# Performance work log

Measured on AMD Instinct MI355X. Metric: run time of the kernel, lower is better.

Reference implementation:

```python
import jax, jax.numpy as jnp
import numpy as np
import math

LN_EPS = 1e-5

def layer_norm(x, g, b):
    mu = jnp.mean(x, axis=-1, keepdims=True)
    var = jnp.mean(jnp.square(x - mu), axis=-1, keepdims=True)
    return (x - mu) * jax.lax.rsqrt(var + LN_EPS) * g + b

def positional_encoding(seq_len, d_model):
    pos = jnp.arange(seq_len, dtype=jnp.float32)[:, None]
    div = jnp.exp(jnp.arange(0, d_model, 2, dtype=jnp.float32) * (-math.log(10000.0) / d_model))
    ang = pos * div  # [S, D/2]
    # interleave: even indices sin, odd indices cos
    return jnp.stack([jnp.sin(ang), jnp.cos(ang)], axis=-1).reshape(seq_len, d_model)

def setup_inputs() -> dict:
    key = jax.random.key(0)
    V, D, H, L, F, B, S = 32000, 768, 12, 6, 3072, 4, 1024
    ks = jax.random.split(key, 12)
    s = 0.02
    inp = {
        'tokens': jax.random.randint(ks[0], (B, S), 0, V),
        'emb': jax.random.normal(ks[1], (V, D), jnp.float32) * s,
        'Wq': jax.random.normal(ks[2], (L, D, D), jnp.float32) * s,
        'bq': jnp.zeros((L, D), jnp.float32),
        'Wk': jax.random.normal(ks[3], (L, D, D), jnp.float32) * s,
        'bk': jnp.zeros((L, D), jnp.float32),
        'Wv': jax.random.normal(ks[4], (L, D, D), jnp.float32) * s,
        'bv': jnp.zeros((L, D), jnp.float32),
        'Wo': jax.random.normal(ks[5], (L, D, D), jnp.float32) * s,
        'bo': jnp.zeros((L, D), jnp.float32),
        'W1': jax.random.normal(ks[6], (L, D, F), jnp.float32) * s,
        'b1': jnp.zeros((L, F), jnp.float32),
        'W2': jax.random.normal(ks[7], (L, F, D), jnp.float32) * s,
        'b2': jnp.zeros((L, D), jnp.float32),
        'ln1_g': jnp.ones((L, D), jnp.float32), 'ln1_b': jnp.zeros((L, D), jnp.float32),
        'ln2_g': jnp.ones((L, D), jnp.float32), 'ln2_b': jnp.zeros((L, D), jnp.float32),
        'lnf_g': jnp.ones((D,), jnp.float32), 'lnf_b': jnp.zeros((D,), jnp.float32),
        'head_W': jax.random.normal(ks[8], (V, D), jnp.float32) * s,
    }
    return inp

def gpt_forward(tokens, emb, Wq, bq, Wk, bk, Wv, bv, Wo, bo, W1, b1, W2, b2,
                ln1_g, ln1_b, ln2_g, ln2_b, lnf_g, lnf_b, head_W):
    B, S = tokens.shape
    D = emb.shape[1]
    H = 12
    dk = D // H
    scale = 1.0 / math.sqrt(dk)
    causal = jnp.tril(jnp.ones((S, S), dtype=bool))  # [S,S]

    x = emb[tokens] + positional_encoding(S, D)  # [B,S,D]

    def block(x, p):
        wq, bq_, wk, bk_, wv, bv_, wo, bo_, w1, b1_, w2, b2_, g1, be1, g2, be2 = p
        h = layer_norm(x, g1, be1)
        q = (h @ wq + bq_).reshape(B, S, H, dk)
        k = (h @ wk + bk_).reshape(B, S, H, dk)
        v = (h @ wv + bv_).reshape(B, S, H, dk)
        scores = jnp.einsum('bqhd,bkhd->bhqk', q, k) * scale
        scores = jnp.where(causal, scores, -jnp.inf)
        attn = jax.nn.softmax(scores, axis=-1)
        o = jnp.einsum('bhqk,bkhd->bqhd', attn, v).reshape(B, S, D)
        x = x + o @ wo + bo_
        h2 = layer_norm(x, g2, be2)
        ff = jax.nn.gelu(h2 @ w1 + b1_, approximate=False) @ w2 + b2_
        x = x + ff
        return x, None

    layer_params = (Wq, bq, Wk, bk, Wv, bv, Wo, bo, W1, b1, W2, b2,
                    ln1_g, ln1_b, ln2_g, ln2_b)
    x, _ = jax.lax.scan(block, x, layer_params)
    x = layer_norm(x, lnf_g, lnf_b)
    logits = jnp.einsum('bsd,vd->bsv', x, head_W)  # head bias=False
    return logits

def reference(tokens, emb, Wq, bq, Wk, bk, Wv, bv, Wo, bo, W1, b1, W2, b2,
              ln1_g, ln1_b, ln2_g, ln2_b, lnf_g, lnf_b, head_W):
    return gpt_forward(tokens, emb, Wq, bq, Wk, bk, Wv, bv, Wo, bo, W1, b1, W2, b2,
                       ln1_g, ln1_b, ln2_g, ln2_b, lnf_g, lnf_b, head_W)
```

## Files before the change

kernel.cpp:

```cpp
#include <hip/hip_runtime.h>
#include <hip/hip_bf16.h>
#include <math.h>

#define BB 4
#define SS 1024
#define DD 768
#define HH 12
#define LL 6
#define FF 3072
#define VV 32000
#define DK 64
#define MM (BB * SS)

typedef __attribute__((ext_vector_type(8))) short s8v;
typedef __attribute__((ext_vector_type(4))) float f4v;

__device__ inline unsigned short f2bf_bits(float f) {
    unsigned u = __builtin_bit_cast(unsigned, f);
    unsigned r = (u + 0x7fffu + ((u >> 16) & 1u)) >> 16;
    return (unsigned short)r;
}

__device__ inline void gl_lds16(const void* g, void* l) {
    __builtin_amdgcn_global_load_lds((const __attribute__((address_space(1))) void*)g,
                                     (__attribute__((address_space(3))) void*)l, 16, 0, 0);
}

__global__ void embed_kernel(const int* __restrict__ tokens,
                             const float* __restrict__ emb,
                             float* __restrict__ x) {
    const int row = blockIdx.x;
    const int s = row % SS;
    const int tok = tokens[row];
    const float* er = emb + (size_t)tok * DD;
    float* xr = x + (size_t)row * DD;
    const float neg_ln_base = -logf(10000.0f) / (float)DD;
    for (int d = threadIdx.x; d < DD; d += blockDim.x) {
        int i2 = d & ~1;
        float div = expf((float)i2 * neg_ln_base);
        float ang = (float)s * div;
        float pe = (d & 1) ? cosf(ang) : sinf(ang);
        xr[d] = er[d] + pe;
    }
}

template <int OUTBF>
__global__ __launch_bounds__(256) void ln_kernel(const float* __restrict__ x,
                                                 const float* __restrict__ g,
                                                 const float* __restrict__ b,
                                                 void* __restrict__ outp) {
    const int row = blockIdx.x;
    const float* xr = x + (size_t)row * DD;
    float s = 0.f, s2 = 0.f;
    for (int d = threadIdx.x; d < DD; d += blockDim.x) {
        float v = xr[d];
        s += v; s2 += v * v;
    }
    __shared__ float rs[4], rs2[4];
    for (int off = 32; off; off >>= 1) {
        s  += __shfl_down(s, off);
        s2 += __shfl_down(s2, off);
    }
    const int wid = threadIdx.x >> 6;
    if ((threadIdx.x & 63) == 0) { rs[wid] = s; rs2[wid] = s2; }
    __syncthreads();
    s  = rs[0] + rs[1] + rs[2] + rs[3];
    s2 = rs2[0] + rs2[1] + rs2[2] + rs2[3];
    const float mu = s / (float)DD;
    const float var = s2 / (float)DD - mu * mu;
    const float r = rsqrtf(var + 1e-5f);
    for (int d = threadIdx.x; d < DD; d += blockDim.x) {
        float v = (xr[d] - mu) * r * g[d] + b[d];
        if (OUTBF) ((unsigned short*)outp)[(size_t)row * DD + d] = f2bf_bits(v);
        else       ((float*)outp)[(size_t)row * DD + d] = v;
    }
}

__global__ __launch_bounds__(256) void prep_kernel(const float* __restrict__ Wq,
                                                   const float* __restrict__ Wk,
                                                   const float* __restrict__ Wv,
                                                   const float* __restrict__ Wo,
                                                   const float* __restrict__ W1,
                                                   const float* __restrict__ W2,
                                                   unsigned short* __restrict__ wqkvT,
                                                   unsigned short* __restrict__ woT,
                                                   unsigned short* __restrict__ w1T,
                                                   unsigned short* __restrict__ w2T) {
    const int id = blockIdx.x;
    const float* src; unsigned short* dst; int R, C, t;
    if (id < 432)       { int seg = id / 144; t = id % 144;
                          src = (seg == 0 ? Wq : seg == 1 ? Wk : Wv);
                          dst = wqkvT + (size_t)seg * DD * DD; R = DD; C = DD; }
    else if (id < 576)  { t = id - 576 + 144; src = Wo; dst = woT; R = DD; C = DD; }
    else if (id < 1152) { t = id - 576;  src = W1; dst = w1T; R = DD; C = FF; }
    else                { t = id - 1152; src = W2; dst = w2T; R = FF; C = DD; }
    const int tilesC = C / 64;
    const int r0 = (t / tilesC) * 64, c0 = (t % tilesC) * 64;
    __shared__ float tb[64][65];
    const int lr = threadIdx.x >> 6, lc = threadIdx.x & 63;
    #pragma unroll
    for (int it = 0; it < 16; ++it) {
        int r = it * 4 + lr;
        tb[r][lc] = src[(size_t)(r0 + r) * C + c0 + lc];
    }
    __syncthreads();
    #pragma unroll
    for (int it = 0; it < 16; ++it) {
        int c = it * 4 + lr;
        dst[(size_t)(c0 + c) * R + r0 + lc] = f2bf_bits(tb[lc][c]);
    }
}

__global__ __launch_bounds__(256) void conv_kernel(const float* __restrict__ in,
                                                   unsigned short* __restrict__ out,
                                                   long n4) {
    long i = (long)blockIdx.x * 256 + threadIdx.x;
    if (i < n4) {
        float4 v = ((const float4*)in)[i];
        ushort4 o;
        o.x = f2bf_bits(v.x); o.y = f2bf_bits(v.y);
        o.z = f2bf_bits(v.z); o.w = f2bf_bits(v.w);
        ((ushort4*)out)[i] = o;
    }
}

template <int ACT, int RES, int OUTMODE>
__global__ __launch_bounds__(256) void gemm_mfma(const unsigned short* __restrict__ A,
                                                 const unsigned short* __restrict__ Bt,
                                                 const float* __restrict__ bias,
                                                 const float* res,
                                                 void* Cout, int M, int N, int K,
                                                 const float* biasK, const float* biasV,
                                                 unsigned short* kout, unsigned short* vtout) {
    __shared__ unsigned short As[128 * 32];
    __shared__ unsigned short Bs[128 * 32];
    const int tid = threadIdx.x;
    const int bm = blockIdx.y * 128, bn = blockIdx.x * 128;
    const int lane = tid & 63;
    const int wave = tid >> 6;
    const int wm = (wave >> 1) * 64, wn = (wave & 1) * 64;

    f4v acc[4][4];
    #pragma unroll
    for (int i = 0; i < 4; i++)
        #pragma unroll
        for (int j = 0; j < 4; j++)
            acc[i][j] = (f4v){0.f, 0.f, 0.f, 0.f};

    const int arow = tid >> 2;
    const int acol = (tid & 3) * 8;
    const unsigned short* gA0 = A  + (size_t)(bm + arow) * K + acol;
    const unsigned short* gA1 = gA0 + (size_t)64 * K;
    const unsigned short* gB0 = Bt + (size_t)(bn + arow) * K + acol;
    const unsigned short* gB1 = gB0 + (size_t)64 * K;
    char* lA0 = (char*)As + tid * 16;
    char* lA1 = lA0 + 4096;
    char* lB0 = (char*)Bs + tid * 16;
    char* lB1 = lB0 + 4096;

    const int fr = lane & 15;
    const int fk = (lane >> 4) * 8;

    for (int k0 = 0; k0 < K; k0 += 32) {
        gl_lds16(gA0 + k0, lA0);
        gl_lds16(gA1 + k0, lA1);
        gl_lds16(gB0 + k0, lB0);
        gl_lds16(gB1 + k0, lB1);
        __syncthreads();
        s8v af[4], bf[4];
        #pragma unroll
        for (int i = 0; i < 4; i++)
            af[i] = *(const s8v*)(As + (wm + i * 16 + fr) * 32 + fk);
        #pragma unroll
        for (int j = 0; j < 4; j++)
            bf[j] = *(const s8v*)(Bs + (wn + j * 16 + fr) * 32 + fk);
        #pragma unroll
        for (int i = 0; i < 4; i++)
            #pragma unroll
            for (int j = 0; j < 4; j++)
                acc[i][j] = __builtin_amdgcn_mfma_f32_16x16x32_bf16(af[i], bf[j], acc[i][j], 0, 0, 0);
        __syncthreads();
    }

    const int r0 = bm + wm + (lane >> 4) * 4;
    const int c0 = bn + wn + fr;
    #pragma unroll
    for (int i = 0; i < 4; i++) {
        const int rb = r0 + i * 16;
        #pragma unroll
        for (int j = 0; j < 4; j++) {
            const int c = c0 + j * 16;
            if (OUTMODE == 3) {
                const int seg = (c >= 1536) ? 2 : (c >= 768 ? 1 : 0);
                const int cc = c - seg * 768;
                const float bb = (seg == 0 ? bias[cc] : seg == 1 ? biasK[cc] : biasV[cc]);
                if (seg < 2) {
                    unsigned short* dst = (seg == 0 ? (unsigned short*)Cout : kout);
                    #pragma unroll
                    for (int q = 0; q < 4; q++)
                        dst[(size_t)(rb + q) * DD + cc] = f2bf_bits(acc[i][j][q] + bb);
                } else {
                    const int b_ = rb / SS, s_ = rb % SS;
                    const int h_ = cc >> 6, dd = cc & 63;
                    ushort4 pk;
                    pk.x = f2bf_bits(acc[i][j][0] + bb);
                    pk.y = f2bf_bits(acc[i][j][1] + bb);
                    pk.z = f2bf_bits(acc[i][j][2] + bb);
                    pk.w = f2bf_bits(acc[i][j][3] + bb);
                    *(ushort4*)(vtout + ((size_t)(b_ * HH + h_) * DK + dd) * SS + s_) = pk;
                }
            } else {
                const float bv = bias ? bias[c] : 0.f;
                #pragma unroll
                for (int q = 0; q < 4; q++) {
                    const int r = rb + q;
                    float v = acc[i][j][q] + bv;
                    if (ACT) v = 0.5f * v * (1.0f + erff(v * 0.70710678118654752f));
                    if (RES) v += res[(size_t)r * N + c];
                    if (OUTMODE == 1) ((unsigned short*)Cout)[(size_t)r * N + c] = f2bf_bits(v);
                    else              ((float*)Cout)[(size_t)r * N + c] = v;
                }
            }
        }
    }
}

__global__ __launch_bounds__(256) void fattn_kernel(const unsigned short* __restrict__ qb,
                                                    const unsigned short* __restrict__ kb,
                                                    const unsigned short* __restrict__ vt,
                                                    unsigned short* __restrict__ o) {
    __shared__ unsigned short Ks[64 * 64];
    __shared__ unsigned short Vs[64 * 64];
    __shared__ unsigned short Ps[4][16 * 64];

    const int qt = (int)gridDim.x - 1 - (int)blockIdx.x;
    const int bh = blockIdx.y;
    const int b = bh / HH, h = bh % HH;
    const int tid = threadIdx.x;
    const int lane = tid & 63;
    const int w = tid >> 6;
    const int fr = lane & 15;
    const int g  = lane >> 4;

    const int sr = tid >> 3;
    const int sc = tid & 7;
    const int scol = (sc * 8) ^ ((sr & 7) * 8);

    const int q0w = qt * 64 + w * 16;
    s8v qf[2];
    {
        const unsigned short* qrow = qb + (size_t)(b * SS + q0w + fr) * DD + h * DK + g * 8;
        qf[0] = *(const s8v*)(qrow);
        qf[1] = *(const s8v*)(qrow + 32);
    }

    f4v ofr[4];
    #pragma unroll
    for (int dj = 0; dj < 4; dj++) ofr[dj] = (f4v){0.f, 0.f, 0.f, 0.f};
    float mrow[4] = {-1e30f, -1e30f, -1e30f, -1e30f};
    float lrow[4] = {0.f, 0.f, 0.f, 0.f};

    unsigned short* Pw = &Ps[w][0];
    const int ktiles = qt + 1;

    for (int t = 0; t < ktiles; ++t) {
        const int k0 = t * 64;
        #pragma unroll
        for (int i = 0; i < 2; i++) {
            const int r = i * 32 + sr;
            gl_lds16(kb + (size_t)(b * SS + k0 + r) * DD + h * DK + scol,
                     (char*)Ks + i * 4096 + tid * 16);
            gl_lds16(vt + ((size_t)bh * DK + r) * SS + k0 + scol,
                     (char*)Vs + i * 4096 + tid * 16);
        }
        __syncthreads();

        f4v sfr[4];
        #pragma unroll
        for (int j = 0; j < 4; j++) {
            const char* kbase = (const char*)Ks + (j * 16 + fr) * 128;
            s8v b0 = *(const s8v*)(kbase + ((g * 16)      ^ ((fr & 7) << 4)));
            s8v b1 = *(const s8v*)(kbase + ((64 + g * 16) ^ ((fr & 7) << 4)));
            f4v a = (f4v){0.f, 0.f, 0.f, 0.f};
            a = __builtin_amdgcn_mfma_f32_16x16x32_bf16(qf[0], b0, a, 0, 0, 0);
            a = __builtin_amdgcn_mfma_f32_16x16x32_bf16(qf[1], b1, a, 0, 0, 0);
            sfr[j] = a;
        }

        const bool diag = (t == ktiles - 1);
        float p[4][4];
        #pragma unroll
        for (int j = 0; j < 4; j++)
            #pragma unroll
            for (int pq = 0; pq < 4; pq++) {
                float sv = sfr[j][pq] * 0.125f;
                if (diag && (k0 + j * 16 + fr > q0w + g * 4 + pq)) sv = -1e30f;
                p[j][pq] = sv;
            }

        float rmx[4];
        #pragma unroll
        for (int pq = 0; pq < 4; pq++)
            rmx[pq] = fmaxf(fmaxf(p[0][pq], p[1][pq]), fmaxf(p[2][pq], p[3][pq]));
        #pragma unroll
        for (int off = 1; off < 16; off <<= 1)
            #pragma unroll
            for (int pq = 0; pq < 4; pq++)
                rmx[pq] = fmaxf(rmx[pq], __shfl_xor(rmx[pq], off));

        float mnew[4], scf[4], rsum[4];
        #pragma unroll
        for (int pq = 0; pq < 4; pq++) {
            mnew[pq] = fmaxf(mrow[pq], rmx[pq]);
            scf[pq]  = __expf(mrow[pq] - mnew[pq]);
            rsum[pq] = 0.f;
        }
        #pragma unroll
        for (int j = 0; j < 4; j++)
            #pragma unroll
            for (int pq = 0; pq < 4; pq++) {
                float e = __expf(p[j][pq] - mnew[pq]);
                p[j][pq] = e;
                rsum[pq] += e;
            }
        #pragma unroll
        for (int off = 1; off < 16; off <<= 1)
            #pragma unroll
            for (int pq = 0; pq < 4; pq++)
                rsum[pq] += __shfl_xor(rsum[pq], off);
        #pragma unroll
        for (int pq = 0; pq < 4; pq++) {
            lrow[pq] = lrow[pq] * scf[pq] + rsum[pq];
            mrow[pq] = mnew[pq];
        }
        #pragma unroll
        for (int dj = 0; dj < 4; dj++)
            #pragma unroll
            for (int pq = 0; pq < 4; pq++)
                ofr[dj][pq] *= scf[pq];

        #pragma unroll
        for (int j = 0; j < 4; j++)
            #pragma unroll
            for (int pq = 0; pq < 4; pq++) {
                const int r = g * 4 + pq;
                *(unsigned short*)((char*)Pw + r * 128 + ((j * 32 + fr * 2) ^ ((r & 7) << 4))) =
                    f2bf_bits(p[j][pq]);
            }

        s8v pa0 = *(const s8v*)((const char*)Pw + fr * 128 + ((g * 16)       ^ ((fr & 7) << 4)));
        s8v pa1 = *(const s8v*)((const char*)Pw + fr * 128 + ((64 + g * 16)  ^ ((fr & 7) << 4)));
        #pragma unroll
        for (int dj = 0; dj < 4; dj++) {
            const char* vbase = (const char*)Vs + (dj * 16 + fr) * 128;
            s8v v0 = *(const s8v*)(vbase + ((g * 16)      ^ ((fr & 7) << 4)));
            s8v v1 = *(const s8v*)(vbase + ((64 + g * 16) ^ ((fr & 7) << 4)));
            ofr[dj] = __builtin_amdgcn_mfma_f32_16x16x32_bf16(pa0, v0, ofr[dj], 0, 0, 0);
            ofr[dj] = __builtin_amdgcn_mfma_f32_16x16x32_bf16(pa1, v1, ofr[dj], 0, 0, 0);
        }
        __syncthreads();
    }

    #pragma unroll
    for (int pq = 0; pq < 4; pq++) {
        const float inv = 1.0f / lrow[pq];
        const int row_abs = q0w + g * 4 + pq;
        #pragma unroll
        for (int dj = 0; dj < 4; dj++)
            o[(size_t)(b * SS + row_abs) * DD + h * DK + dj * 16 + fr] =
                f2bf_bits(ofr[dj][pq] * inv);
    }
}

extern "C" void kernel_launch(void* const* d_in, const int* in_sizes, int n_in,
                              void* d_out, int out_size, void* d_ws, size_t ws_size,
                              hipStream_t stream) {
    const int*   tokens = (const int*)d_in[0];
    const float* emb    = (const float*)d_in[1];
    const float* Wq     = (const float*)d_in[2];
    const float* bq     = (const float*)d_in[3];
    const float* Wk     = (const float*)d_in[4];
    const float* bk     = (const float*)d_in[5];
    const float* Wv     = (const float*)d_in[6];
    const float* bv     = (const float*)d_in[7];
    const float* Wo     = (const float*)d_in[8];
    const float* bo     = (const float*)d_in[9];
    const float* W1     = (const float*)d_in[10];
    const float* b1     = (const float*)d_in[11];
    const float* W2     = (const float*)d_in[12];
    const float* b2     = (const float*)d_in[13];
    const float* ln1_g  = (const float*)d_in[14];
    const float* ln1_b  = (const float*)d_in[15];
    const float* ln2_g  = (const float*)d_in[16];
    const float* ln2_b  = (const float*)d_in[17];
    const float* lnf_g  = (const float*)d_in[18];
    const float* lnf_b  = (const float*)d_in[19];
    const float* headW  = (const float*)d_in[20];
    float* out = (float*)d_out;
    (void)in_sizes; (void)n_in; (void)out_size; (void)ws_size;

    const size_t MD  = (size_t)MM * DD;
    const size_t MF  = (size_t)MM * FF;
    const size_t DxD = (size_t)DD * DD;
    const size_t DxF = (size_t)DD * FF;
    const size_t HWs = (size_t)VV * DD;

    char* p = (char*)d_ws;
    float*          x     = (float*)p;          p += MD * 4;
    unsigned short* qb    = (unsigned short*)p; p += MD * 2;
    unsigned short* kbuf  = (unsigned short*)p; p += MD * 2;
    unsigned short* vtb   = (unsigned short*)p; p += MD * 2;
    unsigned short* ao    = (unsigned short*)p; p += MD * 2;
    unsigned short* h     = (unsigned short*)p; p += MD * 2;
    unsigned short* mid   = (unsigned short*)p; p += MF * 2;
    unsigned short* wqkvT = (unsigned short*)p; p += 3 * DxD * 2;
    unsigned short* woT   = (unsigned short*)p; p += DxD * 2;
    unsigned short* w1T   = (unsigned short*)p; p += DxF * 2;
    unsigned short* w2T   = (unsigned short*)p; p += DxF * 2;
    unsigned short* hw    = (unsigned short*)p; p += HWs * 2;

    embed_kernel<<<MM, 256, 0, stream>>>(tokens, emb, x);
    conv_kernel<<<(int)((HWs / 4 + 255) / 256), 256, 0, stream>>>(headW, hw, (long)(HWs / 4));

    const dim3 gQKV(2304 / 128, MM / 128);
    const dim3 gD(DD * 2 / 256, MM / 128);
    const dim3 gF(FF / 128, MM / 128);
    const dim3 gV(VV / 128, MM / 128);
    const dim3 gA(SS / 64, BB * HH);

    for (int l = 0; l < LL; l++) {
        prep_kernel<<<1728, 256, 0, stream>>>(Wq + l * DxD, Wk + l * DxD, Wv + l * DxD,
                                              Wo + l * DxD, W1 + l * DxF, W2 + l * DxF,
                                              wqkvT, woT, w1T, w2T);
        ln_kernel<1><<<MM, 256, 0, stream>>>(x, ln1_g + l * DD, ln1_b + l * DD, h);
        gemm_mfma<0, 0, 3><<<gQKV, 256, 0, stream>>>(h, wqkvT, bq + l * DD, nullptr, qb,
                                                     MM, 2304, DD,
                                                     bk + l * DD, bv + l * DD, kbuf, vtb);
        fattn_kernel<<<gA, 256, 0, stream>>>(qb, kbuf, vtb, ao);
        gemm_mfma<0, 1, 0><<<gD, 256, 0, stream>>>(ao, woT, bo + l * DD, x, x, MM, DD, DD,
                                                   nullptr, nullptr, nullptr, nullptr);
        ln_kernel<1><<<MM, 256, 0, stream>>>(x, ln2_g + l * DD, ln2_b + l * DD, h);
        gemm_mfma<1, 0, 1><<<gF, 256, 0, stream>>>(h, w1T, b1 + l * FF, nullptr, mid,
                                                   MM, FF, DD, nullptr, nullptr, nullptr, nullptr);
        gemm_mfma<0, 1, 0><<<gD, 256, 0, stream>>>(mid, w2T, b2 + l * DD, x, x, MM, DD, FF,
                                                   nullptr, nullptr, nullptr, nullptr);
    }

    ln_kernel<1><<<MM, 256, 0, stream>>>(x, lnf_g, lnf_b, h);
    gemm_mfma<0, 0, 0><<<gV, 256, 0, stream>>>(h, hw, nullptr, nullptr, out, MM, VV, DD,
                                               nullptr, nullptr, nullptr, nullptr);
}
```

Measured before the change: 2.023 ms.

## Add dedicated 256x128 head GEMM and widen attention key tiles to 128

Adds a separate kernel for the large vocabulary projection. It uses 512 threads, 256x128 output tiles, a workgroup-id swizzle across groups of 8 and nontemporal stores for the large fp32 logits output. The flash-attention kernel now processes 128 keys per iteration instead of 64. That halves the loop trips and barriers per query tile, at the cost of more LDS and registers per block. The head kernel is single-buffered with K-step 32, so it relies on occupancy to hide load latency.

After: 1.870 ms. 7.6% less time.

```diff
diff --git a/kernel.cpp b/kernel.cpp
--- a/kernel.cpp
+++ b/kernel.cpp
@@ -225,13 +225,89 @@
     }
 }
 
+__global__ __launch_bounds__(512) void gemm_head(const unsigned short* __restrict__ A,
+                                                 const unsigned short* __restrict__ Bt,
+                                                 float* __restrict__ C,
+                                                 int M, int N, int K) {
+    __shared__ unsigned short As[256 * 32];
+    __shared__ unsigned short Bs[128 * 32];
+    const int tid = threadIdx.x;
+
+    const int nwg = gridDim.x * gridDim.y;
+    const int bid = blockIdx.y * gridDim.x + blockIdx.x;
+    const int cpx = nwg >> 3;
+    const int swz = (bid & 7) * cpx + (bid >> 3);
+    const int bx = swz % gridDim.x;
+    const int by = swz / gridDim.x;
+    const int bm = by * 256, bn = bx * 128;
+
+    const int lane = tid & 63;
+    const int wave = tid >> 6;
+    const int wm = (wave >> 1) * 64;
+    const int wn = (wave & 1) * 64;
+
+    f4v acc[4][4];
+    #pragma unroll
+    for (int i = 0; i < 4; i++)
+        #pragma unroll
+        for (int j = 0; j < 4; j++)
+            acc[i][j] = (f4v){0.f, 0.f, 0.f, 0.f};
+
+    const int arow = tid >> 2;
+    const int acol = (tid & 3) * 8;
+    const unsigned short* gA0 = A  + (size_t)(bm + arow) * K + acol;
+    const unsigned short* gA1 = gA0 + (size_t)128 * K;
+    const unsigned short* gB  = Bt + (size_t)(bn + arow) * K + acol;
+    char* lA0 = (char*)As + tid * 16;
+    char* lA1 = lA0 + 8192;
+    char* lB  = (char*)Bs + tid * 16;
+
+    const int fr = lane & 15;
+    const int fk = (lane >> 4) * 8;
+
+    for (int k0 = 0; k0 < K; k0 += 32) {
+        gl_lds16(gA0 + k0, lA0);
+        gl_lds16(gA1 + k0, lA1);
+        gl_lds16(gB + k0, lB);
+        __syncthreads();
+        s8v af[4], bf[4];
+        #pragma unroll
+        for (int i = 0; i < 4; i++)
+            af[i] = *(const s8v*)(As + (wm + i * 16 + fr) * 32 + fk);
+        #pragma unroll
+        for (int j = 0; j < 4; j++)
+            bf[j] = *(const s8v*)(Bs + (wn + j * 16 + fr) * 32 + fk);
+        #pragma unroll
+        for (int i = 0; i < 4; i++)
+            #pragma unroll
+            for (int j = 0; j < 4; j++)
+                acc[i][j] = __builtin_amdgcn_mfma_f32_16x16x32_bf16(af[i], bf[j], acc[i][j], 0, 0, 0);
+        __syncthreads();
+    }
+
+    const int r0 = bm + wm + (lane >> 4) * 4;
+    const int c0 = bn + wn + fr;
+    #pragma unroll
+    for (int i = 0; i < 4; i++) {
+        #pragma unroll
+        for (int j = 0; j < 4; j++) {
+            const int c = c0 + j * 16;
+            #pragma unroll
+            for (int q = 0; q < 4; q++) {
+                const int r = r0 + i * 16 + q;
+                __builtin_nontemporal_store(acc[i][j][q], &C[(size_t)r * N + c]);
+            }
+        }
+    }
+}
+
 __global__ __launch_bounds__(256) void fattn_kernel(const unsigned short* __restrict__ qb,
                                                     const unsigned short* __restrict__ kb,
                                                     const unsigned short* __restrict__ vt,
                                                     unsigned short* __restrict__ o) {
-    __shared__ unsigned short Ks[64 * 64];
-    __shared__ unsigned short Vs[64 * 64];
-    __shared__ unsigned short Ps[4][16 * 64];
+    __shared__ unsigned short Ks[128 * 64];
+    __shared__ unsigned short Vs[64 * 128];
+    __shared__ unsigned short Ps[4][16 * 128];
 
     const int qt = (int)gridDim.x - 1 - (int)blockIdx.x;
     const int bh = blockIdx.y;
@@ -242,9 +318,10 @@
     const int fr = lane & 15;
     const int g  = lane >> 4;
 
-    const int sr = tid >> 3;
-    const int sc = tid & 7;
-    const int scol = (sc * 8) ^ ((sr & 7) * 8);
+    const int krow_ = tid >> 3;
+    const int kcol = (((tid & 7) ^ (krow_ & 7)) * 8);
+    const int vrow_ = tid >> 4;
+    const int vcol = (((tid & 15) ^ (vrow_ & 7)) * 8);
 
     const int q0w = qt * 64 + w * 16;
     s8v qf[2];
@@ -261,47 +338,49 @@
     float lrow[4] = {0.f, 0.f, 0.f, 0.f};
 
     unsigned short* Pw = &Ps[w][0];
-    const int ktiles = qt + 1;
+    const int ktiles = qt / 2 + 1;
 
     for (int t = 0; t < ktiles; ++t) {
-        const int k0 = t * 64;
-        #pragma unroll
-        for (int i = 0; i < 2; i++) {
-            const int r = i * 32 + sr;
-            gl_lds16(kb + (size_t)(b * SS + k0 + r) * DD + h * DK + scol,
+        const int k0 = t * 128;
+        #pragma unroll
+        for (int i = 0; i < 4; i++) {
+            const int r = i * 32 + krow_;
+            gl_lds16(kb + (size_t)(b * SS + k0 + r) * DD + h * DK + kcol,
                      (char*)Ks + i * 4096 + tid * 16);
-            gl_lds16(vt + ((size_t)bh * DK + r) * SS + k0 + scol,
+        }
+        #pragma unroll
+        for (int i = 0; i < 4; i++) {
+            const int d = i * 16 + vrow_;
+            gl_lds16(vt + ((size_t)bh * DK + d) * SS + k0 + vcol,
                      (char*)Vs + i * 4096 + tid * 16);
         }
         __syncthreads();
 
-        f4v sfr[4];
-        #pragma unroll
-        for (int j = 0; j < 4; j++) {
+        const bool diag = (t == ktiles - 1);
+        float p[8][4];
+        #pragma unroll
+        for (int j = 0; j < 8; j++) {
             const char* kbase = (const char*)Ks + (j * 16 + fr) * 128;
             s8v b0 = *(const s8v*)(kbase + ((g * 16)      ^ ((fr & 7) << 4)));
             s8v b1 = *(const s8v*)(kbase + ((64 + g * 16) ^ ((fr & 7) << 4)));
             f4v a = (f4v){0.f, 0.f, 0.f, 0.f};
             a = __builtin_amdgcn_mfma_f32_16x16x32_bf16(qf[0], b0, a, 0, 0, 0);
             a = __builtin_amdgcn_mfma_f32_16x16x32_bf16(qf[1], b1, a, 0, 0, 0);
-            sfr[j] = a;
-        }
-
-        const bool diag = (t == ktiles - 1);
-        float p[4][4];
-        #pragma unroll
-        for (int j = 0; j < 4; j++)
             #pragma unroll
             for (int pq = 0; pq < 4; pq++) {
-                float sv = sfr[j][pq] * 0.125f;
+                float sv = a[pq] * 0.125f;
                 if (diag && (k0 + j * 16 + fr > q0w + g * 4 + pq)) sv = -1e30f;
                 p[j][pq] = sv;
             }
+        }
 
         float rmx[4];
         #pragma unroll
-        for (int pq = 0; pq < 4; pq++)
-            rmx[pq] = fmaxf(fmaxf(p[0][pq], p[1][pq]), fmaxf(p[2][pq], p[3][pq]));
+        for (int pq = 0; pq < 4; pq++) {
+            float v0 = fmaxf(fmaxf(p[0][pq], p[1][pq]), fmaxf(p[2][pq], p[3][pq]));
+            float v1 = fmaxf(fmaxf(p[4][pq], p[5][pq]), fmaxf(p[6][pq], p[7][pq]));
+            rmx[pq] = fmaxf(v0, v1);
+        }
         #pragma unroll
         for (int off = 1; off < 16; off <<= 1)
             #pragma unroll
@@ -316,7 +395,7 @@
             rsum[pq] = 0.f;
         }
         #pragma unroll
-        for (int j = 0; j < 4; j++)
+        for (int j = 0; j < 8; j++)
             #pragma unroll
             for (int pq = 0; pq < 4; pq++) {
                 float e = __expf(p[j][pq] - mnew[pq]);
@@ -340,23 +419,27 @@
                 ofr[dj][pq] *= scf[pq];
 
         #pragma unroll
-        for (int j = 0; j < 4; j++)
+        for (int j = 0; j < 8; j++)
             #pragma unroll
             for (int pq = 0; pq < 4; pq++) {
                 const int r = g * 4 + pq;
-                *(unsigned short*)((char*)Pw + r * 128 + ((j * 32 + fr * 2) ^ ((r & 7) << 4))) =
-                    f2bf_bits(p[j][pq]);
+                *(unsigned short*)((char*)Pw + r * 256 +
+                                   (((j * 16 + fr) * 2) ^ ((r & 7) << 4))) = f2bf_bits(p[j][pq]);
             }
 
-        s8v pa0 = *(const s8v*)((const char*)Pw + fr * 128 + ((g * 16)       ^ ((fr & 7) << 4)));
-        s8v pa1 = *(const s8v*)((const char*)Pw + fr * 128 + ((64 + g * 16)  ^ ((fr & 7) << 4)));
+        s8v pa[4];
+        #pragma unroll
+        for (int ks = 0; ks < 4; ks++)
+            pa[ks] = *(const s8v*)((const char*)Pw + fr * 256 +
+                                   ((ks * 64 + g * 16) ^ ((fr & 7) << 4)));
         #pragma unroll
         for (int dj = 0; dj < 4; dj++) {
-            const char* vbase = (const char*)Vs + (dj * 16 + fr) * 128;
-            s8v v0 = *(const s8v*)(vbase + ((g * 16)      ^ ((fr & 7) << 4)));
-            s8v v1 = *(const s8v*)(vbase + ((64 + g * 16) ^ ((fr & 7) << 4)));
-            ofr[dj] = __builtin_amdgcn_mfma_f32_16x16x32_bf16(pa0, v0, ofr[dj], 0, 0, 0);
-            ofr[dj] = __builtin_amdgcn_mfma_f32_16x16x32_bf16(pa1, v1, ofr[dj], 0, 0, 0);
+            const char* vbase = (const char*)Vs + (dj * 16 + fr) * 256;
+            #pragma unroll
+            for (int ks = 0; ks < 4; ks++) {
+                s8v vv = *(const s8v*)(vbase + ((ks * 64 + g * 16) ^ ((fr & 7) << 4)));
+                ofr[dj] = __builtin_amdgcn_mfma_f32_16x16x32_bf16(pa[ks], vv, ofr[dj], 0, 0, 0);
+            }
         }
         __syncthreads();
     }
@@ -423,9 +506,9 @@
     conv_kernel<<<(int)((HWs / 4 + 255) / 256), 256, 0, stream>>>(headW, hw, (long)(HWs / 4));
 
     const dim3 gQKV(2304 / 128, MM / 128);
-    const dim3 gD(DD * 2 / 256, MM / 128);
+    const dim3 gD(DD / 128, MM / 128);
     const dim3 gF(FF / 128, MM / 128);
-    const dim3 gV(VV / 128, MM / 128);
+    const dim3 gHead(VV / 128, MM / 256);
     const dim3 gA(SS / 64, BB * HH);
 
     for (int l = 0; l < LL; l++) {
@@ -447,6 +530,5 @@
     }
 
     ln_kernel<1><<<MM, 256, 0, stream>>>(x, lnf_g, lnf_b, h);
-    gemm_mfma<0, 0, 0><<<gV, 256, 0, stream>>>(h, hw, nullptr, nullptr, out, MM, VV, DD,
-                                               nullptr, nullptr, nullptr, nullptr);
-}
+    gemm_head<<<gHead, 512, 0, stream>>>(h, hw, out, MM, VV, DD);
+}
```
